# Optimization experiments

Hardware: AMD Instinct MI355X
Metric: run time of the kernel (lower is better)

Reference implementation:

```python
import jax, jax.numpy as jnp
import numpy as np

B, L, V, E, U = 128, 64, 50000, 256, 256  # units = lstm_dim/2 = 256


def setup_inputs() -> dict:
    key = jax.random.key(0)
    ks = jax.random.split(key, 12)
    iq = jax.random.randint(ks[0], (B, L), 0, V, dtype=jnp.int32)
    ir = jax.random.randint(ks[1], (B, L), 0, V, dtype=jnp.int32)
    ql = jax.random.randint(ks[2], (B,), 1, L + 1, dtype=jnp.int32)
    rl = jax.random.randint(ks[3], (B,), 1, L + 1, dtype=jnp.int32)
    # all off-diagonal (i, j) pairs in row-major order (negative mask = 1 - eye)
    qi, ri = np.nonzero(1 - np.eye(B, dtype=np.int32))
    return {
        "input_queries": iq, "input_replies": ir,
        "query_lengths": ql, "reply_lengths": rl,
        "neg_q_idx": jnp.asarray(qi, jnp.int32), "neg_r_idx": jnp.asarray(ri, jnp.int32),
        "embeddings": jax.random.normal(ks[4], (V, E), jnp.float32) * 0.02,
        "gate_k": jax.random.normal(ks[5], (4, 2, E + U, 2 * U), jnp.float32) * 0.05,
        "gate_b": jnp.ones((4, 2, 2 * U), jnp.float32),
        "cand_k": jax.random.normal(ks[6], (4, 2, E + U, U), jnp.float32) * 0.05,
        "cand_b": jnp.zeros((4, 2, U), jnp.float32),
        "w1": jax.random.normal(ks[7], (4 * 4 * U + 1, 1024), jnp.float32) * 0.02,
        "b1": jnp.zeros((1024,), jnp.float32),
        "w2": jax.random.normal(ks[8], (1024, 2), jnp.float32) * 0.05,
        "b2": jnp.zeros((2,), jnp.float32),
    }


def _gru(x, h, k, b, kc, bc):
    # TF GRUCell: r,u = sigmoid([x,h]@k + b); c = tanh([x, r*h]@kc + bc); h' = u*h + (1-u)*c
    rz = jax.nn.sigmoid(jnp.concatenate([x, h], 1) @ k + b)
    r, z = jnp.split(rz, 2, axis=1)
    c = jnp.tanh(jnp.concatenate([x, r * h], 1) @ kc + bc)
    return z * h + (1.0 - z) * c


def _encode(emb, lengths, gk, gb, ck, cb):
    # 2-layer stacked GRU over time with sequence-length masking; returns concat of
    # both layers' final states ([B, 2U]) as in MultiRNNCell + dynamic_rnn.
    b, l, _ = emb.shape
    mask = jnp.arange(l)[None, :] < lengths[:, None]  # [B, L]

    def step(carry, inp):
        h1, h2 = carry
        x, m = inp
        h1n = _gru(x, h1, gk[0], gb[0], ck[0], cb[0])
        h2n = _gru(h1n, h2, gk[1], gb[1], ck[1], cb[1])
        m = m[:, None]
        return (jnp.where(m, h1n, h1), jnp.where(m, h2n, h2)), None

    init = (jnp.zeros((b, U), emb.dtype), jnp.zeros((b, U), emb.dtype))
    (h1, h2), _ = jax.lax.scan(step, init, (emb.transpose(1, 0, 2), mask.T))
    return jnp.concatenate([h1, h2], axis=1)


def _rev_seq(emb, lengths):
    # per-row reversal of the first `length` timesteps (tf.reverse_sequence)
    t = jnp.arange(emb.shape[1])[None, :]
    idx = jnp.where(t < lengths[:, None], lengths[:, None] - 1 - t, t)
    return jnp.take_along_axis(emb, idx[:, :, None], axis=1)


def reference(input_queries, input_replies, query_lengths, reply_lengths,
              neg_q_idx, neg_r_idx, embeddings, gate_k, gate_b, cand_k, cand_b,
              w1, b1, w2, b2):
    qe = embeddings[input_queries]  # [B, L, E]
    re_ = embeddings[input_replies]
    q_fw = _encode(qe, query_lengths, gate_k[0], gate_b[0], cand_k[0], cand_b[0])
    q_bw = _encode(_rev_seq(qe, query_lengths), query_lengths,
                   gate_k[1], gate_b[1], cand_k[1], cand_b[1])
    r_fw = _encode(re_, reply_lengths, gate_k[2], gate_b[2], cand_k[2], cand_b[2])
    r_bw = _encode(_rev_seq(re_, reply_lengths), reply_lengths,
                   gate_k[3], gate_b[3], cand_k[3], cand_b[3])
    Q = jnp.concatenate([q_fw, q_bw], 1)  # [B, 4U]
    R = jnp.concatenate([r_fw, r_bw], 1)

    dist = Q @ R.T                                    # [B, B]
    pos_d = jnp.diagonal(dist)[:, None]               # [B, 1]
    neg_d = dist[neg_q_idx, neg_r_idx][:, None]        # [N, 1]
    pos_in = jnp.concatenate([Q, pos_d, Q - R, Q * R, R], 1)
    Qn, Rn = Q[neg_q_idx], R[neg_r_idx]
    neg_in = jnp.concatenate([Qn, neg_d, Qn - Rn, Qn * Rn, Rn], 1)

    x = jnp.concatenate([pos_in, neg_in], 0)           # [B + N, 4*4U + 1]
    h = jax.nn.relu(x @ w1 + b1)
    return h @ w2 + b2                                 # logits [B + N, 2]
```

## Files before the change

kernel.cpp:

```cpp
#include <hip/hip_runtime.h>
#include <hip/hip_fp16.h>
#include <cmath>

typedef _Float16 h2 __attribute__((ext_vector_type(2)));
typedef _Float16 f16x8 __attribute__((ext_vector_type(8)));
typedef float f32x4 __attribute__((ext_vector_type(4)));

#define MFMA16 __builtin_amdgcn_mfma_f32_16x16x32_f16

#if defined(__has_builtin)
#if __has_builtin(__builtin_amdgcn_fdot2)
#define HAS_FDOT2 1
#endif
#endif

__device__ __forceinline__ float fdot2f(h2 a, h2 b, float c) {
#ifdef HAS_FDOT2
    return __builtin_amdgcn_fdot2(a, b, c, false);
#else
    c = fmaf((float)a[0], (float)b[0], c);
    return fmaf((float)a[1], (float)b[1], c);
#endif
}

__device__ __forceinline__ float sigm(float x) { return 1.0f / (1.0f + expf(-x)); }
__device__ __forceinline__ unsigned short f16b(float x) {
    _Float16 h = (_Float16)x; return __builtin_bit_cast(unsigned short, h);
}

__global__ __launch_bounds__(256) void conv_all(
    const float* __restrict__ gate_k, const float* __restrict__ cand_k,
    const float* __restrict__ w1,
    float* __restrict__ gkh, float* __restrict__ ckh,
    f16x8* __restrict__ wB, float* __restrict__ wcomb)
{
    int i = blockIdx.x * 256 + threadIdx.x;
    if (i < 8 * 256 * 512) {
        int col = i & 511, kp = (i >> 9) & 255, e2 = i >> 17;
        const float* src = gate_k + ((size_t)e2 * 512 + 2 * kp) * 512 + col;
        h2 v; v[0] = (_Float16)src[0]; v[1] = (_Float16)src[512];
        gkh[i] = __builtin_bit_cast(float, v);
    }
    if (i < 8 * 256 * 256) {
        int col = i & 255, kp = (i >> 8) & 255, e2 = i >> 16;
        const float* src = cand_k + ((size_t)e2 * 512 + 2 * kp) * 256 + col;
        h2 v; v[0] = (_Float16)src[0]; v[1] = (_Float16)src[256];
        ckh[i] = __builtin_bit_cast(float, v);
    }
    if (i < 32 * 64 * 64) {
        int l = i & 63, nt = (i >> 6) & 63, kt = i >> 12;
        int k0 = kt*32 + ((l >> 4) << 3);
        int n  = (nt << 4) + (l & 15);
        const float* src = w1 + (size_t)(2049 + k0) * 1024 + n;
        f16x8 v;
        #pragma unroll
        for (int j = 0; j < 8; ++j) v[j] = (_Float16)src[(size_t)j * 1024];
        wB[i] = v;
    }
    {
        int mat = i >> 20;
        int e = i & 1048575;
        const float* wmain = mat ? (w1 + (size_t)3073 * 1024) : w1;
        const float* wdiff = w1 + (size_t)1025 * 1024;
        float sgn = mat ? -1.f : 1.f;
        wcomb[i] = wmain[e] + sgn * wdiff[e];
    }
}

__device__ __forceinline__ void gate_partial_h(
    const _Float16* in0f, float* pbuf, const float* __restrict__ gk, int tid)
{
    int cg = tid & 127, q = tid >> 7;
    int c0 = cg * 4;
    const float* gp = gk + (size_t)(q * 32) * 512 + c0;
    const _Float16* xp = in0f + q * 32 * 8;
    float4 A0 = {0.f,0.f,0.f,0.f}, A1 = {0.f,0.f,0.f,0.f};
    float4 A2 = {0.f,0.f,0.f,0.f}, A3 = {0.f,0.f,0.f,0.f};
    #pragma unroll 8
    for (int i = 0; i < 32; ++i) {
        float4 wf = *(const float4*)(gp + (size_t)i * 512);
        float4 xf = *(const float4*)(xp + i * 8);
        h2 w0 = __builtin_bit_cast(h2, wf.x), w1 = __builtin_bit_cast(h2, wf.y);
        h2 w2 = __builtin_bit_cast(h2, wf.z), w3 = __builtin_bit_cast(h2, wf.w);
        h2 x0 = __builtin_bit_cast(h2, xf.x), x1 = __builtin_bit_cast(h2, xf.y);
        h2 x2 = __builtin_bit_cast(h2, xf.z), x3 = __builtin_bit_cast(h2, xf.w);
        A0.x = fdot2f(x0, w0, A0.x); A0.y = fdot2f(x0, w1, A0.y);
        A0.z = fdot2f(x0, w2, A0.z); A0.w = fdot2f(x0, w3, A0.w);
        A1.x = fdot2f(x1, w0, A1.x); A1.y = fdot2f(x1, w1, A1.y);
        A1.z = fdot2f(x1, w2, A1.z); A1.w = fdot2f(x1, w3, A1.w);
        A2.x = fdot2f(x2, w0, A2.x); A2.y = fdot2f(x2, w1, A2.y);
        A2.z = fdot2f(x2, w2, A2.z); A2.w = fdot2f(x2, w3, A2.w);
        A3.x = fdot2f(x3, w0, A3.x); A3.y = fdot2f(x3, w1, A3.y);
        A3.z = fdot2f(x3, w2, A3.z); A3.w = fdot2f(x3, w3, A3.w);
    }
    *(float4*)&pbuf[(q * 4 + 0) * 512 + c0] = A0;
    *(float4*)&pbuf[(q * 4 + 1) * 512 + c0] = A1;
    *(float4*)&pbuf[(q * 4 + 2) * 512 + c0] = A2;
    *(float4*)&pbuf[(q * 4 + 3) * 512 + c0] = A3;
}

__device__ __forceinline__ void cand_partial_h(
    const _Float16* in0f, float* pbuf, const float* __restrict__ ck, int tid)
{
    int cg = tid & 63, q = tid >> 6;
    int c0 = cg * 4;
    const float* cp = ck + (size_t)(q * 16) * 256 + c0;
    const _Float16* xp = in0f + q * 16 * 8;
    float4 A0 = {0.f,0.f,0.f,0.f}, A1 = {0.f,0.f,0.f,0.f};
    float4 A2 = {0.f,0.f,0.f,0.f}, A3 = {0.f,0.f,0.f,0.f};
    #pragma unroll 8
    for (int i = 0; i < 16; ++i) {
        float4 wf = *(const float4*)(cp + (size_t)i * 256);
        float4 xf = *(const float4*)(xp + i * 8);
        h2 w0 = __builtin_bit_cast(h2, wf.x), w1 = __builtin_bit_cast(h2, wf.y);
        h2 w2 = __builtin_bit_cast(h2, wf.z), w3 = __builtin_bit_cast(h2, wf.w);
        h2 x0 = __builtin_bit_cast(h2, xf.x), x1 = __builtin_bit_cast(h2, xf.y);
        h2 x2 = __builtin_bit_cast(h2, xf.z), x3 = __builtin_bit_cast(h2, xf.w);
        A0.x = fdot2f(x0, w0, A0.x); A0.y = fdot2f(x0, w1, A0.y);
        A0.z = fdot2f(x0, w2, A0.z); A0.w = fdot2f(x0, w3, A0.w);
        A1.x = fdot2f(x1, w0, A1.x); A1.y = fdot2f(x1, w1, A1.y);
        A1.z = fdot2f(x1, w2, A1.z); A1.w = fdot2f(x1, w3, A1.w);
        A2.x = fdot2f(x2, w0, A2.x); A2.y = fdot2f(x2, w1, A2.y);
        A2.z = fdot2f(x2, w2, A2.z); A2.w = fdot2f(x2, w3, A2.w);
        A3.x = fdot2f(x3, w0, A3.x); A3.y = fdot2f(x3, w1, A3.y);
        A3.z = fdot2f(x3, w2, A3.z); A3.w = fdot2f(x3, w3, A3.w);
    }
    *(float4*)&pbuf[(q * 4 + 0) * 256 + c0] = A0;
    *(float4*)&pbuf[(q * 4 + 1) * 256 + c0] = A1;
    *(float4*)&pbuf[(q * 4 + 2) * 256 + c0] = A2;
    *(float4*)&pbuf[(q * 4 + 3) * 256 + c0] = A3;
}

__global__ __launch_bounds__(1024, 4) void gru_encode(
    const int* __restrict__ iq, const int* __restrict__ ir,
    const int* __restrict__ ql, const int* __restrict__ rl,
    const float* __restrict__ emb,
    const float* __restrict__ gkh, const float* __restrict__ gate_b,
    const float* __restrict__ ckh, const float* __restrict__ cand_b,
    float* __restrict__ Qo, float* __restrict__ Ro)
{
    int bid = blockIdx.x;
    int xcd = bid & 7;
    int enc = xcd >> 1;
    int chunk = (xcd & 1) * 16 + (bid >> 3);
    int b0 = chunk * 4;
    int tid = threadIdx.x;
    int c = tid & 255, r = tid >> 8;

    const int* toks = (enc < 2) ? iq : ir;
    const int* lens = (enc < 2) ? ql : rl;
    const bool bw = (enc & 1);

    const float* gk1 = gkh + (size_t)(enc * 2 + 0) * 131072;
    const float* gk2 = gkh + (size_t)(enc * 2 + 1) * 131072;
    const float* gb1 = gate_b + (enc * 2 + 0) * 512;
    const float* gb2 = gate_b + (enc * 2 + 1) * 512;
    const float* ck1 = ckh + (size_t)(enc * 2 + 0) * 65536;
    const float* ck2 = ckh + (size_t)(enc * 2 + 1) * 65536;
    const float* cb1 = cand_b + (enc * 2 + 0) * 256;
    const float* cb2 = cand_b + (enc * 2 + 1) * 256;

    __shared__ __align__(16) _Float16 in0fA[256 * 8];
    __shared__ __align__(16) _Float16 in0fB[256 * 8];
    __shared__ float pbuf[16384];
    __shared__ float h1rt[4][256];
    __shared__ float h2rt[4][256];
    __shared__ float gzt[4][256];
    __shared__ int len_s[4];

    h1rt[r][c] = 0.f;
    h2rt[r][c] = 0.f;
    if (tid < 4) len_s[tid] = lens[b0 + tid];
    __syncthreads();
    int maxlen = max(max(len_s[0], len_s[1]), max(len_s[2], len_s[3]));
    if (tid < 512) {
        int kp = tid >> 2, rr = tid & 3;
        int len = len_s[rr];
        int tok = toks[(b0 + rr) * 64 + (bw ? (len - 1) : 0)];
        float2 xv = *(const float2*)(emb + (size_t)tok * 256 + 2 * kp);
        h2 v; v[0] = (_Float16)xv.x; v[1] = (_Float16)xv.y;
        *(float*)(in0fA + kp * 8 + rr * 2) = __builtin_bit_cast(float, v);
    } else {
        int m = (tid - 512) >> 2, rr = tid & 3;
        *(unsigned int*)(in0fA + (128 + m) * 8 + rr * 2) = 0u;
    }
    __syncthreads();

    for (int t = 0; t < maxlen; ++t) {
        gate_partial_h(in0fA, pbuf, gk1, tid);
        __syncthreads();
        {
            float s0 = gb1[c], s1 = gb1[256 + c];
            #pragma unroll
            for (int q = 0; q < 8; ++q) {
                s0 += pbuf[(q * 4 + r) * 512 + c];
                s1 += pbuf[(q * 4 + r) * 512 + c + 256];
            }
            float rh = sigm(s0) * h1rt[r][c];
            gzt[r][c] = sigm(s1);
            in0fA[((256 + c) >> 1) * 8 + r * 2 + (c & 1)] = (_Float16)rh;
        }
        __syncthreads();
        cand_partial_h(in0fA, pbuf, ck1, tid);
        __syncthreads();
        {
            float s = cb1[c];
            #pragma unroll
            for (int q = 0; q < 16; ++q) s += pbuf[(q * 4 + r) * 256 + c];
            float cv = tanhf(s);
            float z = gzt[r][c];
            float hn = fmaf(z, h1rt[r][c] - cv, cv);
            float hm = (t < len_s[r]) ? hn : h1rt[r][c];
            h1rt[r][c] = hm;
            in0fB[(c >> 1) * 8 + r * 2 + (c & 1)]         = (_Float16)hn;
            in0fB[((256 + c) >> 1) * 8 + r * 2 + (c & 1)] = (_Float16)h2rt[r][c];
            in0fA[((256 + c) >> 1) * 8 + r * 2 + (c & 1)] = (_Float16)hm;
        }
        __syncthreads();

        gate_partial_h(in0fB, pbuf, gk2, tid);
        __syncthreads();
        {
            float s0 = gb2[c], s1 = gb2[256 + c];
            #pragma unroll
            for (int q = 0; q < 8; ++q) {
                s0 += pbuf[(q * 4 + r) * 512 + c];
                s1 += pbuf[(q * 4 + r) * 512 + c + 256];
            }
            float rh = sigm(s0) * h2rt[r][c];
            gzt[r][c] = sigm(s1);
            in0fB[((256 + c) >> 1) * 8 + r * 2 + (c & 1)] = (_Float16)rh;
        }
        __syncthreads();
        cand_partial_h(in0fB, pbuf, ck2, tid);
        __syncthreads();
        {
            float s = cb2[c];
            #pragma unroll
            for (int q = 0; q < 16; ++q) s += pbuf[(q * 4 + r) * 256 + c];
            float cv = tanhf(s);
            float z = gzt[r][c];
            float hn = fmaf(z, h2rt[r][c] - cv, cv);
            if (t < len_s[r]) h2rt[r][c] = hn;
        }
        if (tid < 512) {
            int t2 = t + 1;
            if (t2 < 64) {
                int kp = tid >> 2, rr = tid & 3;
                int len = len_s[rr];
                int tt = bw ? ((t2 < len) ? (len - 1 - t2) : t2) : t2;
                int tok = toks[(b0 + rr) * 64 + tt];
                float2 xv = *(const float2*)(emb + (size_t)tok * 256 + 2 * kp);
                h2 v; v[0] = (_Float16)xv.x; v[1] = (_Float16)xv.y;
                *(float*)(in0fA + kp * 8 + rr * 2) = __builtin_bit_cast(float, v);
            }
        }
        __syncthreads();
    }

    float* outp = (enc < 2) ? Qo : Ro;
    int off = (enc & 1) ? 512 : 0;
    outp[(size_t)(b0 + r) * 1024 + off + c]       = h1rt[r][c];
    outp[(size_t)(b0 + r) * 1024 + off + 256 + c] = h2rt[r][c];
}

__global__ __launch_bounds__(256) void ab_kernel(
    const float* __restrict__ Q, const float* __restrict__ R,
    const float* __restrict__ wcomb, float* __restrict__ A, float* __restrict__ Bv)
{
    int nb = blockIdx.x, rb = blockIdx.y, mat = blockIdx.z;
    int tid = threadIdx.x;
    int n = nb * 256 + tid;
    int r0 = rb * 4;
    const float* src = mat ? R : Q;
    const float* wc  = wcomb + (size_t)mat * 1048576;

    __shared__ float Qs[4][64];
    float acc[4] = {0.f, 0.f, 0.f, 0.f};

    for (int k0 = 0; k0 < 1024; k0 += 64) {
        __syncthreads();
        {
            int rr = tid >> 6, kk = tid & 63;
            Qs[rr][kk] = src[(size_t)(r0 + rr) * 1024 + k0 + kk];
        }
        __syncthreads();
        for (int kk = 0; kk < 64; ++kk) {
            float w = wc[(size_t)(k0 + kk) * 1024 + n];
            #pragma unroll
            for (int r = 0; r < 4; ++r)
                acc[r] = fmaf(Qs[r][kk], w, acc[r]);
        }
    }
    float* dst = mat ? Bv : A;
    #pragma unroll
    for (int r = 0; r < 4; ++r)
        dst[(size_t)(r0 + r) * 1024 + n] = acc[r];
}

__global__ __launch_bounds__(512, 2) void pair_gemm(
    const float* __restrict__ Q, const float* __restrict__ R,
    const float* __restrict__ Aq, const float* __restrict__ Bv,
    const int* __restrict__ nqi, const int* __restrict__ nri,
    const f16x8* __restrict__ wB,
    const float* __restrict__ w1, const float* __restrict__ b1,
    const float* __restrict__ w2, float* __restrict__ partial)
{
    int bm = blockIdx.x, bn = blockIdx.y;
    int tid = threadIdx.x, w = tid >> 6, l = tid & 63;
    __shared__ __align__(16) unsigned short As[4096];
    __shared__ float red[2048];
    __shared__ float dred[4][128];
    __shared__ int qis[128], ris[128];
    __shared__ float dsv[128];
    if (tid < 128) {
        int p = bm*128 + tid;
        int qi = (p < 128) ? p : nqi[p-128];
        int ri = (p < 128) ? p : nri[p-128];
        qis[tid] = qi; ris[tid] = ri;
    }
    __syncthreads();

    int srow = tid & 127, skg = tid >> 7;
    const float* qrow = Q + (size_t)qis[srow]*1024 + skg*8;
    const float* rrow = R + (size_t)ris[srow]*1024 + skg*8;

    float4 qa = *(const float4*)(qrow);
    float4 qb = *(const float4*)(qrow + 4);
    float4 ra = *(const float4*)(rrow);
    float4 rb = *(const float4*)(rrow + 4);

    f32x4 acc[8];
    #pragma unroll
    for (int m = 0; m < 8; ++m) acc[m] = (f32x4){0.f,0.f,0.f,0.f};
    float dacc = 0.f;

    for (int kt = 0; kt < 32; ++kt) {
        float p0 = qa.x*ra.x, p1 = qa.y*ra.y, p2 = qa.z*ra.z, p3 = qa.w*ra.w;
        float p4 = qb.x*rb.x, p5 = qb.y*rb.y, p6 = qb.z*rb.z, p7 = qb.w*rb.w;
        dacc += ((p0 + p1) + (p2 + p3)) + ((p4 + p5) + (p6 + p7));
        f16x8 prod;
        prod[0]=(_Float16)p0; prod[1]=(_Float16)p1;
        prod[2]=(_Float16)p2; prod[3]=(_Float16)p3;
        prod[4]=(_Float16)p4; prod[5]=(_Float16)p5;
        prod[6]=(_Float16)p6; prod[7]=(_Float16)p7;
        __syncthreads();
        ((f16x8*)As)[srow*4 + (skg ^ (srow & 3))] = prod;
        __syncthreads();
        if (kt + 1 < 32) {
            qa = *(const float4*)(qrow + (kt+1)*32);
            qb = *(const float4*)(qrow + (kt+1)*32 + 4);
            ra = *(const float4*)(rrow + (kt+1)*32);
            rb = *(const float4*)(rrow + (kt+1)*32 + 4);
        }
        f16x8 bf = wB[((size_t)kt*64 + bn*8 + w)*64 + l];
        #pragma unroll
        for (int mt = 0; mt < 8; ++mt) {
            f16x8 af = ((const f16x8*)As)[(mt*16 + (l & 15))*4 + ((l >> 4) ^ (l & 3))];
            acc[mt] = MFMA16(af, bf, acc[mt], 0, 0, 0);
        }
    }

    dred[skg][srow] = dacc;
    __syncthreads();
    if (tid < 128)
        dsv[tid] = (dred[0][tid] + dred[1][tid]) + (dred[2][tid] + dred[3][tid]);
    __syncthreads();

    int col = bn*128 + w*16 + (l & 15);
    float wd  = w1[(size_t)1024*1024 + col];
    float b1v = b1[col];
    float w20 = w2[col*2], w21 = w2[col*2 + 1];
    #pragma unroll
    for (int mt = 0; mt < 8; ++mt) {
        float po0[4], po1[4];
        #pragma unroll
        for (int j = 0; j < 4; ++j) {
            int lr = mt*16 + (l >> 4)*4 + j;
            float h = acc[mt][j]
                    + Aq[(size_t)qis[lr]*1024 + col]
                    + Bv[(size_t)ris[lr]*1024 + col]
                    + dsv[lr]*wd + b1v;
            h = fmaxf(h, 0.f);
            po0[j] = h * w20; po1[j] = h * w21;
        }
        #pragma unroll
        for (int s = 1; s < 16; s <<= 1) {
            #pragma unroll
            for (int j = 0; j < 4; ++j) {
                po0[j] += __shfl_xor(po0[j], s, 64);
                po1[j] += __shfl_xor(po1[j], s, 64);
            }
        }
        if ((l & 15) == 0) {
            #pragma unroll
            for (int j = 0; j < 4; ++j) {
                int row = mt*16 + (l >> 4)*4 + j;
                red[(w*128 + row)*2 + 0] = po0[j];
                red[(w*128 + row)*2 + 1] = po1[j];
            }
        }
    }
    __syncthreads();
    if (tid < 256) {
        int row = tid >> 1, cc = tid & 1;
        float s = 0.f;
        #pragma unroll
        for (int ww = 0; ww < 8; ++ww) s += red[(ww*128 + row)*2 + cc];
        partial[((size_t)bn*16384 + bm*128 + row)*2 + cc] = s;
    }
}

__global__ void final_reduce(const float* __restrict__ partial,
                             const float* __restrict__ b2, float* __restrict__ out)
{
    int gidx = blockIdx.x * 256 + threadIdx.x;
    int p = gidx >> 1, c = gidx & 1;
    float s = b2[c];
    #pragma unroll
    for (int nt = 0; nt < 8; ++nt)
        s += partial[((size_t)nt * 16384 + p) * 2 + c];
    out[gidx] = s;
}

extern "C" void kernel_launch(void* const* d_in, const int* in_sizes, int n_in,
                              void* d_out, int out_size, void* d_ws, size_t ws_size,
                              hipStream_t stream) {
    const int*   iq     = (const int*)d_in[0];
    const int*   ir     = (const int*)d_in[1];
    const int*   ql     = (const int*)d_in[2];
    const int*   rl     = (const int*)d_in[3];
    const int*   nqi    = (const int*)d_in[4];
    const int*   nri    = (const int*)d_in[5];
    const float* emb    = (const float*)d_in[6];
    const float* gate_k = (const float*)d_in[7];
    const float* gate_b = (const float*)d_in[8];
    const float* cand_k = (const float*)d_in[9];
    const float* cand_b = (const float*)d_in[10];
    const float* w1     = (const float*)d_in[11];
    const float* b1     = (const float*)d_in[12];
    const float* w2     = (const float*)d_in[13];
    const float* b2     = (const float*)d_in[14];
    float* out = (float*)d_out;
    float* ws  = (float*)d_ws;

    float* Q       = ws;
    float* R       = ws + 131072;
    float* A       = ws + 262144;
    float* Bv      = ws + 393216;
    float* partial = ws + 540672;
    float* gkh     = ws + 1064960;
    float* ckh     = ws + 2113536;
    f16x8* wB      = (f16x8*)(ws + 2637824);
    float* wcomb   = ws + 3162112;

    conv_all<<<8192, 256, 0, stream>>>(gate_k, cand_k, w1, gkh, ckh, wB, wcomb);
    gru_encode<<<128, 1024, 0, stream>>>(iq, ir, ql, rl, emb, gkh, gate_b,
                                         ckh, cand_b, Q, R);
    ab_kernel<<<dim3(4, 32, 2), 256, 0, stream>>>(Q, R, wcomb, A, Bv);
    pair_gemm<<<dim3(128, 8), 512, 0, stream>>>(Q, R, A, Bv, nqi, nri,
                                                wB, w1, b1, w2, partial);
    final_reduce<<<128, 256, 0, stream>>>(partial, b2, out);
}
```

Baseline: 1.334 ms.

## Split GRU encoder across 256 blocks with two sequences per block

Each GRU encoder block now processes 2 batch rows instead of 4, and the grid doubles from 128 to 256 blocks. The packed fp16 input layout, the partial-sum buffer and the thread mapping shrink to match, and the elementwise stages use only 512 of the 1024 threads. The aim is to occupy more CUs during the sequential recurrence and shorten the per-step dot-product loops. In exchange, each block reuses every weight load across fewer rows, so total weight traffic from cache doubles.

```diff
diff --git a/kernel.cpp b/kernel.cpp
--- a/kernel.cpp
+++ b/kernel.cpp
@@ -73,30 +73,22 @@
     int cg = tid & 127, q = tid >> 7;
     int c0 = cg * 4;
     const float* gp = gk + (size_t)(q * 32) * 512 + c0;
-    const _Float16* xp = in0f + q * 32 * 8;
+    const _Float16* xp = in0f + q * 32 * 4;
     float4 A0 = {0.f,0.f,0.f,0.f}, A1 = {0.f,0.f,0.f,0.f};
-    float4 A2 = {0.f,0.f,0.f,0.f}, A3 = {0.f,0.f,0.f,0.f};
     #pragma unroll 8
     for (int i = 0; i < 32; ++i) {
         float4 wf = *(const float4*)(gp + (size_t)i * 512);
-        float4 xf = *(const float4*)(xp + i * 8);
+        float2 xf = *(const float2*)(xp + i * 4);
         h2 w0 = __builtin_bit_cast(h2, wf.x), w1 = __builtin_bit_cast(h2, wf.y);
         h2 w2 = __builtin_bit_cast(h2, wf.z), w3 = __builtin_bit_cast(h2, wf.w);
         h2 x0 = __builtin_bit_cast(h2, xf.x), x1 = __builtin_bit_cast(h2, xf.y);
-        h2 x2 = __builtin_bit_cast(h2, xf.z), x3 = __builtin_bit_cast(h2, xf.w);
         A0.x = fdot2f(x0, w0, A0.x); A0.y = fdot2f(x0, w1, A0.y);
         A0.z = fdot2f(x0, w2, A0.z); A0.w = fdot2f(x0, w3, A0.w);
         A1.x = fdot2f(x1, w0, A1.x); A1.y = fdot2f(x1, w1, A1.y);
         A1.z = fdot2f(x1, w2, A1.z); A1.w = fdot2f(x1, w3, A1.w);
-        A2.x = fdot2f(x2, w0, A2.x); A2.y = fdot2f(x2, w1, A2.y);
-        A2.z = fdot2f(x2, w2, A2.z); A2.w = fdot2f(x2, w3, A2.w);
-        A3.x = fdot2f(x3, w0, A3.x); A3.y = fdot2f(x3, w1, A3.y);
-        A3.z = fdot2f(x3, w2, A3.z); A3.w = fdot2f(x3, w3, A3.w);
-    }
-    *(float4*)&pbuf[(q * 4 + 0) * 512 + c0] = A0;
-    *(float4*)&pbuf[(q * 4 + 1) * 512 + c0] = A1;
-    *(float4*)&pbuf[(q * 4 + 2) * 512 + c0] = A2;
-    *(float4*)&pbuf[(q * 4 + 3) * 512 + c0] = A3;
+    }
+    *(float4*)&pbuf[(q * 2 + 0) * 512 + c0] = A0;
+    *(float4*)&pbuf[(q * 2 + 1) * 512 + c0] = A1;
 }
 
 __device__ __forceinline__ void cand_partial_h(
@@ -105,30 +97,22 @@
     int cg = tid & 63, q = tid >> 6;
     int c0 = cg * 4;
     const float* cp = ck + (size_t)(q * 16) * 256 + c0;
-    const _Float16* xp = in0f + q * 16 * 8;
+    const _Float16* xp = in0f + q * 16 * 4;
     float4 A0 = {0.f,0.f,0.f,0.f}, A1 = {0.f,0.f,0.f,0.f};
-    float4 A2 = {0.f,0.f,0.f,0.f}, A3 = {0.f,0.f,0.f,0.f};
     #pragma unroll 8
     for (int i = 0; i < 16; ++i) {
         float4 wf = *(const float4*)(cp + (size_t)i * 256);
-        float4 xf = *(const float4*)(xp + i * 8);
+        float2 xf = *(const float2*)(xp + i * 4);
         h2 w0 = __builtin_bit_cast(h2, wf.x), w1 = __builtin_bit_cast(h2, wf.y);
         h2 w2 = __builtin_bit_cast(h2, wf.z), w3 = __builtin_bit_cast(h2, wf.w);
         h2 x0 = __builtin_bit_cast(h2, xf.x), x1 = __builtin_bit_cast(h2, xf.y);
-        h2 x2 = __builtin_bit_cast(h2, xf.z), x3 = __builtin_bit_cast(h2, xf.w);
         A0.x = fdot2f(x0, w0, A0.x); A0.y = fdot2f(x0, w1, A0.y);
         A0.z = fdot2f(x0, w2, A0.z); A0.w = fdot2f(x0, w3, A0.w);
         A1.x = fdot2f(x1, w0, A1.x); A1.y = fdot2f(x1, w1, A1.y);
         A1.z = fdot2f(x1, w2, A1.z); A1.w = fdot2f(x1, w3, A1.w);
-        A2.x = fdot2f(x2, w0, A2.x); A2.y = fdot2f(x2, w1, A2.y);
-        A2.z = fdot2f(x2, w2, A2.z); A2.w = fdot2f(x2, w3, A2.w);
-        A3.x = fdot2f(x3, w0, A3.x); A3.y = fdot2f(x3, w1, A3.y);
-        A3.z = fdot2f(x3, w2, A3.z); A3.w = fdot2f(x3, w3, A3.w);
-    }
-    *(float4*)&pbuf[(q * 4 + 0) * 256 + c0] = A0;
-    *(float4*)&pbuf[(q * 4 + 1) * 256 + c0] = A1;
-    *(float4*)&pbuf[(q * 4 + 2) * 256 + c0] = A2;
-    *(float4*)&pbuf[(q * 4 + 3) * 256 + c0] = A3;
+    }
+    *(float4*)&pbuf[(q * 2 + 0) * 256 + c0] = A0;
+    *(float4*)&pbuf[(q * 2 + 1) * 256 + c0] = A1;
 }
 
 __global__ __launch_bounds__(1024, 4) void gru_encode(
@@ -142,10 +126,9 @@
     int bid = blockIdx.x;
     int xcd = bid & 7;
     int enc = xcd >> 1;
-    int chunk = (xcd & 1) * 16 + (bid >> 3);
-    int b0 = chunk * 4;
+    int chunk = (xcd & 1) * 32 + (bid >> 3);
+    int b0 = chunk * 2;
     int tid = threadIdx.x;
-    int c = tid & 255, r = tid >> 8;
 
     const int* toks = (enc < 2) ? iq : ir;
     const int* lens = (enc < 2) ? ql : rl;
@@ -160,108 +143,114 @@
     const float* cb1 = cand_b + (enc * 2 + 0) * 256;
     const float* cb2 = cand_b + (enc * 2 + 1) * 256;
 
-    __shared__ __align__(16) _Float16 in0fA[256 * 8];
-    __shared__ __align__(16) _Float16 in0fB[256 * 8];
-    __shared__ float pbuf[16384];
-    __shared__ float h1rt[4][256];
-    __shared__ float h2rt[4][256];
-    __shared__ float gzt[4][256];
-    __shared__ int len_s[4];
-
-    h1rt[r][c] = 0.f;
-    h2rt[r][c] = 0.f;
-    if (tid < 4) len_s[tid] = lens[b0 + tid];
-    __syncthreads();
-    int maxlen = max(max(len_s[0], len_s[1]), max(len_s[2], len_s[3]));
-    if (tid < 512) {
-        int kp = tid >> 2, rr = tid & 3;
+    __shared__ __align__(16) _Float16 in0fA[256 * 4];
+    __shared__ __align__(16) _Float16 in0fB[256 * 4];
+    __shared__ float pbuf[8192];
+    __shared__ float h1rt[2][256];
+    __shared__ float h2rt[2][256];
+    __shared__ float gzt[2][256];
+    __shared__ int len_s[2];
+
+    if (tid < 512) { int r = tid >> 8, c = tid & 255; h1rt[r][c] = 0.f; h2rt[r][c] = 0.f; }
+    if (tid < 2) len_s[tid] = lens[b0 + tid];
+    __syncthreads();
+    int maxlen = max(len_s[0], len_s[1]);
+    if (tid < 256) {
+        int kp = tid >> 1, rr = tid & 1;
         int len = len_s[rr];
         int tok = toks[(b0 + rr) * 64 + (bw ? (len - 1) : 0)];
         float2 xv = *(const float2*)(emb + (size_t)tok * 256 + 2 * kp);
         h2 v; v[0] = (_Float16)xv.x; v[1] = (_Float16)xv.y;
-        *(float*)(in0fA + kp * 8 + rr * 2) = __builtin_bit_cast(float, v);
-    } else {
-        int m = (tid - 512) >> 2, rr = tid & 3;
-        *(unsigned int*)(in0fA + (128 + m) * 8 + rr * 2) = 0u;
+        *(float*)(in0fA + kp * 4 + rr * 2) = __builtin_bit_cast(float, v);
+    } else if (tid < 512) {
+        int m = (tid - 256) >> 1, rr = tid & 1;
+        *(unsigned int*)(in0fA + (128 + m) * 4 + rr * 2) = 0u;
     }
     __syncthreads();
 
     for (int t = 0; t < maxlen; ++t) {
         gate_partial_h(in0fA, pbuf, gk1, tid);
         __syncthreads();
-        {
+        if (tid < 512) {
+            int c = tid & 255, r = tid >> 8;
             float s0 = gb1[c], s1 = gb1[256 + c];
             #pragma unroll
             for (int q = 0; q < 8; ++q) {
-                s0 += pbuf[(q * 4 + r) * 512 + c];
-                s1 += pbuf[(q * 4 + r) * 512 + c + 256];
+                s0 += pbuf[(q * 2 + r) * 512 + c];
+                s1 += pbuf[(q * 2 + r) * 512 + c + 256];
             }
             float rh = sigm(s0) * h1rt[r][c];
             gzt[r][c] = sigm(s1);
-            in0fA[((256 + c) >> 1) * 8 + r * 2 + (c & 1)] = (_Float16)rh;
+            in0fA[((256 + c) >> 1) * 4 + r * 2 + (c & 1)] = (_Float16)rh;
         }
         __syncthreads();
         cand_partial_h(in0fA, pbuf, ck1, tid);
         __syncthreads();
-        {
+        if (tid < 512) {
+            int c = tid & 255, r = tid >> 8;
             float s = cb1[c];
             #pragma unroll
-            for (int q = 0; q < 16; ++q) s += pbuf[(q * 4 + r) * 256 + c];
+            for (int q = 0; q < 16; ++q) s += pbuf[(q * 2 + r) * 256 + c];
             float cv = tanhf(s);
             float z = gzt[r][c];
             float hn = fmaf(z, h1rt[r][c] - cv, cv);
             float hm = (t < len_s[r]) ? hn : h1rt[r][c];
             h1rt[r][c] = hm;
-            in0fB[(c >> 1) * 8 + r * 2 + (c & 1)]         = (_Float16)hn;
-            in0fB[((256 + c) >> 1) * 8 + r * 2 + (c & 1)] = (_Float16)h2rt[r][c];
-            in0fA[((256 + c) >> 1) * 8 + r * 2 + (c & 1)] = (_Float16)hm;
+            in0fB[(c >> 1) * 4 + r * 2 + (c & 1)]         = (_Float16)hn;
+            in0fB[((256 + c) >> 1) * 4 + r * 2 + (c & 1)] = (_Float16)h2rt[r][c];
+            in0fA[((256 + c) >> 1) * 4 + r * 2 + (c & 1)] = (_Float16)hm;
         }
         __syncthreads();
 
         gate_partial_h(in0fB, pbuf, gk2, tid);
         __syncthreads();
-        {
+        if (tid < 512) {
+            int c = tid & 255, r = tid >> 8;
             float s0 = gb2[c], s1 = gb2[256 + c];
             #pragma unroll
             for (int q = 0; q < 8; ++q) {
-                s0 += pbuf[(q * 4 + r) * 512 + c];
-                s1 += pbuf[(q * 4 + r) * 512 + c + 256];
+                s0 += pbuf[(q * 2 + r) * 512 + c];
+                s1 += pbuf[(q * 2 + r) * 512 + c + 256];
             }
             float rh = sigm(s0) * h2rt[r][c];
             gzt[r][c] = sigm(s1);
-            in0fB[((256 + c) >> 1) * 8 + r * 2 + (c & 1)] = (_Float16)rh;
+            in0fB[((256 + c) >> 1) * 4 + r * 2 + (c & 1)] = (_Float16)rh;
         }
         __syncthreads();
         cand_partial_h(in0fB, pbuf, ck2, tid);
         __syncthreads();
-        {
+        if (tid < 512) {
+            int c = tid & 255, r = tid >> 8;
             float s = cb2[c];
             #pragma unroll
-            for (int q = 0; q < 16; ++q) s += pbuf[(q * 4 + r) * 256 + c];
+            for (int q = 0; q < 16; ++q) s += pbuf[(q * 2 + r) * 256 + c];
             float cv = tanhf(s);
             float z = gzt[r][c];
             float hn = fmaf(z, h2rt[r][c] - cv, cv);
             if (t < len_s[r]) h2rt[r][c] = hn;
         }
-        if (tid < 512) {
+        if (tid < 256) {
             int t2 = t + 1;
             if (t2 < 64) {
-                int kp = tid >> 2, rr = tid & 3;
+                int kp = tid >> 1, rr = tid & 1;
                 int len = len_s[rr];
                 int tt = bw ? ((t2 < len) ? (len - 1 - t2) : t2) : t2;
                 int tok = toks[(b0 + rr) * 64 + tt];
                 float2 xv = *(const float2*)(emb + (size_t)tok * 256 + 2 * kp);
                 h2 v; v[0] = (_Float16)xv.x; v[1] = (_Float16)xv.y;
-                *(float*)(in0fA + kp * 8 + rr * 2) = __builtin_bit_cast(float, v);
+                *(float*)(in0fA + kp * 4 + rr * 2) = __builtin_bit_cast(float, v);
             }
         }
         __syncthreads();
     }
 
-    float* outp = (enc < 2) ? Qo : Ro;
-    int off = (enc & 1) ? 512 : 0;
-    outp[(size_t)(b0 + r) * 1024 + off + c]       = h1rt[r][c];
-    outp[(size_t)(b0 + r) * 1024 + off + 256 + c] = h2rt[r][c];
+    if (tid < 512) {
+        int r = tid >> 8, c = tid & 255;
+        float* outp = (enc < 2) ? Qo : Ro;
+        int off = (enc & 1) ? 512 : 0;
+        outp[(size_t)(b0 + r) * 1024 + off + c]       = h1rt[r][c];
+        outp[(size_t)(b0 + r) * 1024 + off + 256 + c] = h2rt[r][c];
+    }
 }
 
 __global__ __launch_bounds__(256) void ab_kernel(
@@ -455,7 +444,7 @@
     float* wcomb   = ws + 3162112;
 
     conv_all<<<8192, 256, 0, stream>>>(gate_k, cand_k, w1, gkh, ckh, wB, wcomb);
-    gru_encode<<<128, 1024, 0, stream>>>(iq, ir, ql, rl, emb, gkh, gate_b,
+    gru_encode<<<256, 1024, 0, stream>>>(iq, ir, ql, rl, emb, gkh, gate_b,
                                          ckh, cand_b, Q, R);
     ab_kernel<<<dim3(4, 32, 2), 256, 0, stream>>>(Q, R, wcomb, A, Bv);
     pair_gemm<<<dim3(128, 8), 512, 0, stream>>>(Q, R, A, Bv, nqi, nri,
```

After: 1.084 ms. 1.23x faster.
